# Kernel optimization log

Hardware: AMD Instinct MI355X
Metric: run time of the kernel (lower is better)

The kernel has to match this reference:

```python
import jax, jax.numpy as jnp
import numpy as np

N_NODES = 100000
N_EDGES = 6400000
IN_CH = 128
HID = 32


def setup_inputs() -> dict:
    key = jax.random.key(0)
    ks = jax.random.split(key, 12)
    x = jax.random.normal(ks[0], (N_NODES, IN_CH), dtype=jnp.float32)
    edge_index = jax.random.randint(ks[1], (2, N_EDGES), 0, N_NODES, dtype=jnp.int64)
    # Glorot-ish init for weights, zeros for biases (PyG / nn.Linear defaults vary,
    # values are random anyway for a correctness baseline)
    def w(k, fan_in, fan_out):
        s = 1.0 / np.sqrt(fan_in)
        return jax.random.uniform(k, (fan_in, fan_out), jnp.float32, -s, s)
    return {
        "x": x,
        "edge_index": edge_index,
        "W1": w(ks[2], IN_CH, HID), "b1": jnp.zeros((HID,), jnp.float32),
        "W2": w(ks[3], HID, HID),   "b2": jnp.zeros((HID,), jnp.float32),
        "Wl1": w(ks[4], HID, HID),  "bl1": jnp.zeros((HID,), jnp.float32),
        "Wl2": w(ks[5], HID, 1),    "bl2": jnp.zeros((1,), jnp.float32),
    }


def gcn_conv(x, W, b, src, dst, n_nodes):
    # GCNConv: h = x @ W; add self-loops; symmetric normalization D^-1/2 A_hat D^-1/2;
    # aggregate messages from src into dst; add bias.
    h = x @ W  # [N, out]
    loop = jnp.arange(n_nodes, dtype=src.dtype)
    src2 = jnp.concatenate([src, loop])
    dst2 = jnp.concatenate([dst, loop])
    ones = jnp.ones(src2.shape[0], dtype=h.dtype)
    deg = jax.ops.segment_sum(ones, dst2, num_segments=n_nodes)  # [N]
    dinv = jnp.where(deg > 0, jax.lax.rsqrt(deg), 0.0)
    norm = dinv[src2] * dinv[dst2]  # [E+N]
    msg = h[src2] * norm[:, None]   # [E+N, out]  (dominant memory traffic)
    out = jax.ops.segment_sum(msg, dst2, num_segments=n_nodes)
    return out + b


def reference(x, edge_index, W1, b1, W2, b2, Wl1, bl1, Wl2, bl2):
    src, dst = edge_index[0], edge_index[1]
    n = x.shape[0]
    h = jax.nn.relu(gcn_conv(x, W1, b1, src, dst, n))
    h = jax.nn.relu(gcn_conv(h, W2, b2, src, dst, n))
    h = jax.nn.relu(h @ Wl1 + bl1)
    return h @ Wl2 + bl2  # [N, 1]
```

## Files before the change

kernel.cpp:

```cpp
#include <hip/hip_runtime.h>

#define N_NODES 100000
#define N_EDGES 6400000
#define IN_CH   128
#define HID     32

#define BKT_SHIFT 9
#define BKT_MASK  511
#define BKT_SZ    512
#define NBKT      196
#define NBLK      1024
#define TILE      6250
#define QMAX      8704

#define O_EBUF 0u
#define O_HS   0u
#define O_HS2  12800000u
#define O_GH   25600000u
#define O_CUR  26402816u
#define O_CSR  26402816u
#define O_ROWS 52002816u
#define O_BST  52402824u
#define O_BTOT 52403616u
#define O_FLAG 52404400u

__global__ void k_detect(const unsigned int* e, int* flag) {
    __shared__ int any;
    if (threadIdx.x == 0) any = 0;
    __syncthreads();
    int acc = 0;
    for (int i = threadIdx.x; i < 4096; i += 256)
        acc |= (e[2 * i + 1] != 0u);
    if (acc) atomicOr(&any, 1);
    __syncthreads();
    if (threadIdx.x == 0) *flag = any ? 0 : 1;
}

__device__ __forceinline__ int eload_nt(const int* e, int is64, long long idx) {
    return is64 ? (int)__builtin_nontemporal_load((const long long*)e + idx)
                : __builtin_nontemporal_load(e + (size_t)idx);
}

__global__ void k_hist(const int* e, const int* flag, int* ghist) {
    __shared__ int h[NBKT];
    for (int i = threadIdx.x; i < NBKT; i += 256) h[i] = 0;
    __syncthreads();
    int is64 = *flag;
    long long base = (long long)blockIdx.x * TILE;
    for (int k = threadIdx.x; k < TILE; k += 256) {
        int dst = eload_nt(e, is64, (long long)N_EDGES + base + k);
        atomicAdd(&h[dst >> BKT_SHIFT], 1);
    }
    __syncthreads();
    int* g = ghist + blockIdx.x * NBKT;
    for (int i = threadIdx.x; i < NBKT; i += 256) g[i] = h[i];
}

__global__ void k_scan1(const int* __restrict__ ghist, int* __restrict__ btot) {
    int j = blockIdx.x;
    int t = threadIdx.x;
    int s = 0;
    for (int blk = t; blk < NBLK; blk += 64) s += ghist[blk * NBKT + j];
#pragma unroll
    for (int off = 32; off; off >>= 1) s += __shfl_down(s, off, 64);
    if (t == 0) btot[j] = s;
}

__global__ void k_scan2(const int* __restrict__ btot, int* __restrict__ bstart) {
    __shared__ int s[1024];
    int t = threadIdx.x;
    int v = (t < NBKT) ? btot[t] : 0;
    s[t] = v;
    __syncthreads();
    for (int off = 1; off < 1024; off <<= 1) {
        int u = (t >= off) ? s[t - off] : 0;
        __syncthreads();
        s[t] += u;
        __syncthreads();
    }
    if (t < NBKT) bstart[t] = s[t] - v;
    if (t == 0) bstart[NBKT] = N_EDGES;
}

__global__ void k_scan3(const int* __restrict__ ghist, const int* __restrict__ bstart,
                        int* __restrict__ cursors) {
    int j = blockIdx.x * 256 + threadIdx.x;
    if (j >= NBKT) return;
    int run = bstart[j];
    for (int blk = 0; blk < NBLK; ++blk) {
        cursors[blk * NBKT + j] = run;
        run += ghist[blk * NBKT + j];
    }
}

__launch_bounds__(512)
__global__ void k_scatter(const int* e, const int* flag,
                          const int* __restrict__ ghist, const int* __restrict__ cursors,
                          unsigned int* __restrict__ ebuf) {
    __shared__ unsigned obuf[TILE];
    __shared__ unsigned char bid[TILE];
    __shared__ int lcur[NBKT];
    __shared__ int gbase[NBKT];
    __shared__ int wsum[8];
    int t = threadIdx.x;
    int blk = blockIdx.x;
    {
        int v = (t < NBKT) ? ghist[blk * NBKT + t] : 0;
        int lane = t & 63, w = t >> 6;
        int p = v;
#pragma unroll
        for (int off = 1; off < 64; off <<= 1) {
            int u = __shfl_up(p, off, 64);
            if (lane >= off) p += u;
        }
        if (lane == 63) wsum[w] = p;
        __syncthreads();
        int woff = 0;
        for (int k = 0; k < w; ++k) woff += wsum[k];
        int excl = woff + p - v;
        if (t < NBKT) {
            lcur[t]  = excl;
            gbase[t] = cursors[blk * NBKT + t] - excl;
        }
    }
    __syncthreads();
    int is64 = *flag;
    long long base = (long long)blk * TILE;
    for (int k = t; k < TILE; k += 512) {
        int src = eload_nt(e, is64, base + k);
        int dst = eload_nt(e, is64, (long long)N_EDGES + base + k);
        int b = dst >> BKT_SHIFT;
        int pos = atomicAdd(&lcur[b], 1);
        obuf[pos] = ((unsigned)src << BKT_SHIFT) | (unsigned)(dst & BKT_MASK);
        bid[pos] = (unsigned char)b;
    }
    __syncthreads();
    for (int i = t; i < TILE; i += 512) {
        int b = bid[i];
        ebuf[gbase[b] + i] = obuf[i];
    }
}

__launch_bounds__(512)
__global__ void k_sort2a(const unsigned int* __restrict__ ebuf, const int* __restrict__ bstart,
                         unsigned short* __restrict__ gh2) {
    __shared__ int hist[BKT_SZ];
    int b = blockIdx.x >> 2, q = blockIdx.x & 3;
    int s0 = bstart[b], e0 = bstart[b + 1], len = e0 - s0;
    int lo = s0 + (int)((long long)len * q / 4);
    int hi = s0 + (int)((long long)len * (q + 1) / 4);
    hist[threadIdx.x] = 0;
    __syncthreads();
    for (int i = lo + (int)threadIdx.x; i < hi; i += 512)
        atomicAdd(&hist[__builtin_nontemporal_load(&ebuf[i]) & BKT_MASK], 1);
    __syncthreads();
    gh2[(b * 4 + q) * BKT_SZ + threadIdx.x] = (unsigned short)hist[threadIdx.x];
}

__launch_bounds__(512)
__global__ void k_sort2b(const unsigned int* __restrict__ ebuf, const int* __restrict__ bstart,
                         const unsigned short* __restrict__ gh2, int* __restrict__ csr,
                         int* __restrict__ rows) {
    __shared__ unsigned obuf[QMAX];
    __shared__ unsigned short bid[QMAX];
    __shared__ int lcur[BKT_SZ];
    __shared__ int gbase[BKT_SZ];
    __shared__ int wsA[8], wsB[8];
    int b = blockIdx.x >> 2, q = blockIdx.x & 3;
    int s0 = bstart[b], e0 = bstart[b + 1], len = e0 - s0;
    int lo = s0 + (int)((long long)len * q / 4);
    int hi = s0 + (int)((long long)len * (q + 1) / 4);
    int t = threadIdx.x;
    int h0 = gh2[(b * 4 + 0) * BKT_SZ + t];
    int h1 = gh2[(b * 4 + 1) * BKT_SZ + t];
    int h2 = gh2[(b * 4 + 2) * BKT_SZ + t];
    int h3 = gh2[(b * 4 + 3) * BKT_SZ + t];
    int tot = h0 + h1 + h2 + h3;
    int hq = (q == 0) ? h0 : (q == 1) ? h1 : (q == 2) ? h2 : h3;
    int lane = t & 63, w = t >> 6;
    int p1 = tot, p2 = hq;
#pragma unroll
    for (int off = 1; off < 64; off <<= 1) {
        int u1 = __shfl_up(p1, off, 64);
        int u2 = __shfl_up(p2, off, 64);
        if (lane >= off) { p1 += u1; p2 += u2; }
    }
    if (lane == 63) { wsA[w] = p1; wsB[w] = p2; }
    __syncthreads();
    int woffA = 0, woffB = 0;
    for (int k = 0; k < w; ++k) { woffA += wsA[k]; woffB += wsB[k]; }
    int binstart = s0 + woffA + p1 - tot;
    int lexcl    = woffB + p2 - hq;
    int qs = binstart + ((q > 0) ? h0 : 0) + ((q > 1) ? h1 : 0) + ((q > 2) ? h2 : 0);
    lcur[t]  = lexcl;
    gbase[t] = qs - lexcl;
    int node = b * BKT_SZ + t;
    if (q == 0 && node <= N_NODES) rows[node] = binstart;
    __syncthreads();
    for (int i = lo + t; i < hi; i += 512) {
        unsigned v = __builtin_nontemporal_load(&ebuf[i]);
        int bin = v & BKT_MASK;
        int pos = atomicAdd(&lcur[bin], 1);
        obuf[pos] = v >> BKT_SHIFT;
        bid[pos] = (unsigned short)bin;
    }
    __syncthreads();
    int qlen = hi - lo;
    for (int i = t; i < qlen; i += 512) {
        int bn = bid[i];
        csr[gbase[bn] + i] = (int)obuf[i];
    }
}

__launch_bounds__(256)
__global__ void k_gemm1(const float* __restrict__ x, const float* __restrict__ W1,
                        const int* __restrict__ rows, float* __restrict__ hs) {
    __shared__ float w[IN_CH * HID];
    __shared__ float xs[8 * IN_CH];
    for (int i = threadIdx.x; i < IN_CH * HID; i += 256) w[i] = W1[i];
    const float4* xb = (const float4*)(x + (size_t)blockIdx.x * 8 * IN_CH);
    ((float4*)xs)[threadIdx.x] = xb[threadIdx.x];
    __syncthreads();
    int lane = threadIdx.x & 31, hw = threadIdx.x >> 5;
    int node = blockIdx.x * 8 + hw;
    float dv = rsqrtf((float)(rows[node + 1] - rows[node] + 1));
    const float* xr = xs + hw * IN_CH;
    float acc = 0.f;
#pragma unroll
    for (int k = 0; k < IN_CH; ++k) acc += xr[k] * w[k * HID + lane];
    hs[(size_t)node * HID + lane] = acc * dv;
}

__device__ __forceinline__ float gather_row(const float* __restrict__ feat,
                                            const int* __restrict__ cs,
                                            int len, int lane, float acc) {
    int j = 0;
    for (; j + 16 <= len; j += 16) {
        int idx[16];
#pragma unroll
        for (int u = 0; u < 16; ++u) idx[u] = cs[j + u];
        float f[16];
#pragma unroll
        for (int u = 0; u < 16; ++u) f[u] = feat[(size_t)idx[u] * HID + lane];
        acc += (((f[0] + f[1]) + (f[2] + f[3])) + ((f[4] + f[5]) + (f[6] + f[7])))
             + (((f[8] + f[9]) + (f[10] + f[11])) + ((f[12] + f[13]) + (f[14] + f[15])));
    }
    for (; j + 8 <= len; j += 8) {
        int idx[8];
#pragma unroll
        for (int u = 0; u < 8; ++u) idx[u] = cs[j + u];
        float f[8];
#pragma unroll
        for (int u = 0; u < 8; ++u) f[u] = feat[(size_t)idx[u] * HID + lane];
        acc += ((f[0] + f[1]) + (f[2] + f[3])) + ((f[4] + f[5]) + (f[6] + f[7]));
    }
    for (; j < len; ++j) acc += feat[(size_t)cs[j] * HID + lane];
    return acc;
}

__launch_bounds__(256)
__global__ void k_agg1(const float* __restrict__ hs, const int* __restrict__ csr,
                       const int* __restrict__ rows, const float* __restrict__ b1,
                       const float* __restrict__ W2, float* __restrict__ hs2) {
    __shared__ float w2[HID * HID];
    __shared__ float h1s[8][HID];
    for (int i = threadIdx.x; i < HID * HID; i += 256) w2[i] = W2[i];
    int lane = threadIdx.x & 31, hw = threadIdx.x >> 5;
    int node = blockIdx.x * 8 + hw;
    int r0 = rows[node], r1 = rows[node + 1];
    float dv = rsqrtf((float)(r1 - r0 + 1));
    float acc = hs[(size_t)node * HID + lane];
    acc = gather_row(hs, csr + r0, r1 - r0, lane, acc);
    h1s[hw][lane] = fmaxf(acc * dv + b1[lane], 0.f);
    __syncthreads();
    float g = 0.f;
#pragma unroll
    for (int k = 0; k < HID; ++k) g += h1s[hw][k] * w2[k * HID + lane];
    hs2[(size_t)node * HID + lane] = g * dv;
}

__launch_bounds__(256)
__global__ void k_agg2(const float* __restrict__ hs2, const int* __restrict__ csr,
                       const int* __restrict__ rows, const float* __restrict__ b2,
                       const float* __restrict__ Wl1, const float* __restrict__ bl1,
                       const float* __restrict__ Wl2, const float* __restrict__ bl2,
                       float* __restrict__ out) {
    __shared__ float wl1[HID * HID];
    __shared__ float h2s[8][HID];
    for (int i = threadIdx.x; i < HID * HID; i += 256) wl1[i] = Wl1[i];
    int lane = threadIdx.x & 31, hw = threadIdx.x >> 5;
    int node = blockIdx.x * 8 + hw;
    int r0 = rows[node], r1 = rows[node + 1];
    float dv = rsqrtf((float)(r1 - r0 + 1));
    float acc = hs2[(size_t)node * HID + lane];
    acc = gather_row(hs2, csr + r0, r1 - r0, lane, acc);
    float h2 = fmaxf(acc * dv + b2[lane], 0.f);
    h2s[hw][lane] = h2;
    __syncthreads();
    float g = bl1[lane];
#pragma unroll
    for (int k = 0; k < HID; ++k) g += h2s[hw][k] * wl1[k * HID + lane];
    float o = fmaxf(g, 0.f) * Wl2[lane];
#pragma unroll
    for (int off = 16; off; off >>= 1) o += __shfl_down(o, off, 32);
    if (lane == 0) out[node] = o + *bl2;
}

extern "C" void kernel_launch(void* const* d_in, const int* in_sizes, int n_in,
                              void* d_out, int out_size, void* d_ws, size_t ws_size,
                              hipStream_t stream) {
    const float* x   = (const float*)d_in[0];
    const int*   e   = (const int*)d_in[1];
    const float* W1  = (const float*)d_in[2];
    const float* b1  = (const float*)d_in[3];
    const float* W2  = (const float*)d_in[4];
    const float* b2  = (const float*)d_in[5];
    const float* Wl1 = (const float*)d_in[6];
    const float* bl1 = (const float*)d_in[7];
    const float* Wl2 = (const float*)d_in[8];
    const float* bl2 = (const float*)d_in[9];
    float* out = (float*)d_out;

    char* w = (char*)d_ws;
    unsigned int*   ebuf    = (unsigned int*)(w + O_EBUF);
    float*          hs      = (float*)(w + O_HS);
    float*          hs2     = (float*)(w + O_HS2);
    int*            ghist   = (int*)(w + O_GH);
    unsigned short* gh2     = (unsigned short*)(w + O_GH);
    int*            cursors = (int*)(w + O_CUR);
    int*            csr     = (int*)(w + O_CSR);
    int*            rows    = (int*)(w + O_ROWS);
    int*            bstart  = (int*)(w + O_BST);
    int*            btot    = (int*)(w + O_BTOT);
    int*            flag    = (int*)(w + O_FLAG);

    const int NB_NODE = N_NODES / 8;

    k_detect<<<1, 256, 0, stream>>>((const unsigned int*)e, flag);
    k_hist<<<NBLK, 256, 0, stream>>>(e, flag, ghist);
    k_scan1<<<NBKT, 64, 0, stream>>>(ghist, btot);
    k_scan2<<<1, 1024, 0, stream>>>(btot, bstart);
    k_scan3<<<1, 256, 0, stream>>>(ghist, bstart, cursors);
    k_scatter<<<NBLK, 512, 0, stream>>>(e, flag, ghist, cursors, ebuf);
    k_sort2a<<<NBKT * 4, 512, 0, stream>>>(ebuf, bstart, gh2);
    k_sort2b<<<NBKT * 4, 512, 0, stream>>>(ebuf, bstart, gh2, csr, rows);

    k_gemm1<<<NB_NODE, 256, 0, stream>>>(x, W1, rows, hs);
    k_agg1<<<NB_NODE, 256, 0, stream>>>(hs, csr, rows, b1, W2, hs2);
    k_agg2<<<NB_NODE, 256, 0, stream>>>(hs2, csr, rows, b2,
                                        Wl1, bl1, Wl2, bl2, out);
}
```

Measured before the change: 373.8 us.

## Split aggregation into four 8-channel passes over quarter-sized feature tables

Feature matrices are now stored as four channel slices of 8 floats per node (3.2 MB each) instead of 32-float rows. Each aggregation runs four passes, one per slice, so the gathered table is small enough to stay cache-resident. Each pass uses 8 lanes per edge and 8 edges per wave, followed by a shuffle reduction. The GEMM stages are split out into separate kernels that write the sliced layout. The trade-off is that the CSR index array is read four times per layer, there are more kernel launches, and each gather is only 32 bytes wide.

```diff
diff --git a/kernel.cpp b/kernel.cpp
--- a/kernel.cpp
+++ b/kernel.cpp
@@ -4,6 +4,7 @@
 #define N_EDGES 6400000
 #define IN_CH   128
 #define HID     32
+#define QT      800000
 
 #define BKT_SHIFT 9
 #define BKT_MASK  511
@@ -14,8 +15,8 @@
 #define QMAX      8704
 
 #define O_EBUF 0u
-#define O_HS   0u
-#define O_HS2  12800000u
+#define O_A0   0u
+#define O_A1   12800000u
 #define O_GH   25600000u
 #define O_CUR  26402816u
 #define O_CSR  26402816u
@@ -214,9 +215,10 @@
 
 __launch_bounds__(256)
 __global__ void k_gemm1(const float* __restrict__ x, const float* __restrict__ W1,
-                        const int* __restrict__ rows, float* __restrict__ hs) {
+                        const int* __restrict__ rows, float* __restrict__ hsq) {
     __shared__ float w[IN_CH * HID];
     __shared__ float xs[8 * IN_CH];
+    __shared__ float hstage[8][HID];
     for (int i = threadIdx.x; i < IN_CH * HID; i += 256) w[i] = W1[i];
     const float4* xb = (const float4*)(x + (size_t)blockIdx.x * 8 * IN_CH);
     ((float4*)xs)[threadIdx.x] = xb[threadIdx.x];
@@ -228,74 +230,81 @@
     float acc = 0.f;
 #pragma unroll
     for (int k = 0; k < IN_CH; ++k) acc += xr[k] * w[k * HID + lane];
-    hs[(size_t)node * HID + lane] = acc * dv;
-}
-
-__device__ __forceinline__ float gather_row(const float* __restrict__ feat,
-                                            const int* __restrict__ cs,
-                                            int len, int lane, float acc) {
-    int j = 0;
-    for (; j + 16 <= len; j += 16) {
-        int idx[16];
-#pragma unroll
-        for (int u = 0; u < 16; ++u) idx[u] = cs[j + u];
-        float f[16];
-#pragma unroll
-        for (int u = 0; u < 16; ++u) f[u] = feat[(size_t)idx[u] * HID + lane];
-        acc += (((f[0] + f[1]) + (f[2] + f[3])) + ((f[4] + f[5]) + (f[6] + f[7])))
-             + (((f[8] + f[9]) + (f[10] + f[11])) + ((f[12] + f[13]) + (f[14] + f[15])));
-    }
-    for (; j + 8 <= len; j += 8) {
-        int idx[8];
-#pragma unroll
-        for (int u = 0; u < 8; ++u) idx[u] = cs[j + u];
-        float f[8];
-#pragma unroll
-        for (int u = 0; u < 8; ++u) f[u] = feat[(size_t)idx[u] * HID + lane];
-        acc += ((f[0] + f[1]) + (f[2] + f[3])) + ((f[4] + f[5]) + (f[6] + f[7]));
-    }
-    for (; j < len; ++j) acc += feat[(size_t)cs[j] * HID + lane];
-    return acc;
+    hstage[hw][lane] = acc * dv;
+    __syncthreads();
+    int q = threadIdx.x >> 6, k2 = threadIdx.x & 63;
+    hsq[(size_t)q * QT + blockIdx.x * 64 + k2] = hstage[k2 >> 3][q * 8 + (k2 & 7)];
+}
+
+__launch_bounds__(512)
+__global__ void k_aggpass(const float* __restrict__ tq, const int* __restrict__ csr,
+                          const int* __restrict__ rows, const float* __restrict__ bias,
+                          float* __restrict__ outq) {
+    __shared__ float stage[8][8];
+    int tid = threadIdx.x;
+    int wv = tid >> 6, lane = tid & 63;
+    int eg = lane >> 3, c = lane & 7;
+    int node = blockIdx.x * 8 + wv;
+    int r0 = rows[node], r1 = rows[node + 1];
+    float dv = rsqrtf((float)(r1 - r0 + 1));
+    float acc = 0.f;
+    int j = r0 + eg;
+    for (; j + 24 < r1; j += 32) {
+        int i0 = __builtin_nontemporal_load(csr + j);
+        int i1 = __builtin_nontemporal_load(csr + j + 8);
+        int i2 = __builtin_nontemporal_load(csr + j + 16);
+        int i3 = __builtin_nontemporal_load(csr + j + 24);
+        float f0 = tq[i0 * 8 + c];
+        float f1 = tq[i1 * 8 + c];
+        float f2 = tq[i2 * 8 + c];
+        float f3 = tq[i3 * 8 + c];
+        acc += (f0 + f1) + (f2 + f3);
+    }
+    for (; j < r1; j += 8)
+        acc += tq[__builtin_nontemporal_load(csr + j) * 8 + c];
+#pragma unroll
+    for (int off = 8; off < 64; off <<= 1)
+        acc += __shfl_xor(acc, off, 64);
+    acc += tq[node * 8 + c];
+    float v = fmaxf(acc * dv + bias[c], 0.f);
+    if (lane < 8) stage[wv][c] = v;
+    __syncthreads();
+    if (tid < 64)
+        __builtin_nontemporal_store(stage[tid >> 3][tid & 7],
+                                    outq + (size_t)blockIdx.x * 64 + tid);
 }
 
 __launch_bounds__(256)
-__global__ void k_agg1(const float* __restrict__ hs, const int* __restrict__ csr,
-                       const int* __restrict__ rows, const float* __restrict__ b1,
-                       const float* __restrict__ W2, float* __restrict__ hs2) {
+__global__ void k_gemm2(const float* __restrict__ h1q, const float* __restrict__ W2,
+                        const int* __restrict__ rows, float* __restrict__ hs2q) {
     __shared__ float w2[HID * HID];
     __shared__ float h1s[8][HID];
+    __shared__ float hstage[8][HID];
     for (int i = threadIdx.x; i < HID * HID; i += 256) w2[i] = W2[i];
     int lane = threadIdx.x & 31, hw = threadIdx.x >> 5;
     int node = blockIdx.x * 8 + hw;
-    int r0 = rows[node], r1 = rows[node + 1];
-    float dv = rsqrtf((float)(r1 - r0 + 1));
-    float acc = hs[(size_t)node * HID + lane];
-    acc = gather_row(hs, csr + r0, r1 - r0, lane, acc);
-    h1s[hw][lane] = fmaxf(acc * dv + b1[lane], 0.f);
-    __syncthreads();
+    h1s[hw][lane] = h1q[(size_t)(lane >> 3) * QT + node * 8 + (lane & 7)];
+    __syncthreads();
+    float dv = rsqrtf((float)(rows[node + 1] - rows[node] + 1));
     float g = 0.f;
 #pragma unroll
     for (int k = 0; k < HID; ++k) g += h1s[hw][k] * w2[k * HID + lane];
-    hs2[(size_t)node * HID + lane] = g * dv;
+    hstage[hw][lane] = g * dv;
+    __syncthreads();
+    int q = threadIdx.x >> 6, k2 = threadIdx.x & 63;
+    hs2q[(size_t)q * QT + blockIdx.x * 64 + k2] = hstage[k2 >> 3][q * 8 + (k2 & 7)];
 }
 
 __launch_bounds__(256)
-__global__ void k_agg2(const float* __restrict__ hs2, const int* __restrict__ csr,
-                       const int* __restrict__ rows, const float* __restrict__ b2,
-                       const float* __restrict__ Wl1, const float* __restrict__ bl1,
-                       const float* __restrict__ Wl2, const float* __restrict__ bl2,
-                       float* __restrict__ out) {
+__global__ void k_head(const float* __restrict__ h2q, const float* __restrict__ Wl1,
+                       const float* __restrict__ bl1, const float* __restrict__ Wl2,
+                       const float* __restrict__ bl2, float* __restrict__ out) {
     __shared__ float wl1[HID * HID];
     __shared__ float h2s[8][HID];
     for (int i = threadIdx.x; i < HID * HID; i += 256) wl1[i] = Wl1[i];
     int lane = threadIdx.x & 31, hw = threadIdx.x >> 5;
     int node = blockIdx.x * 8 + hw;
-    int r0 = rows[node], r1 = rows[node + 1];
-    float dv = rsqrtf((float)(r1 - r0 + 1));
-    float acc = hs2[(size_t)node * HID + lane];
-    acc = gather_row(hs2, csr + r0, r1 - r0, lane, acc);
-    float h2 = fmaxf(acc * dv + b2[lane], 0.f);
-    h2s[hw][lane] = h2;
+    h2s[hw][lane] = h2q[(size_t)(lane >> 3) * QT + node * 8 + (lane & 7)];
     __syncthreads();
     float g = bl1[lane];
 #pragma unroll
@@ -322,17 +331,17 @@
     float* out = (float*)d_out;
 
     char* w = (char*)d_ws;
-    unsigned int*   ebuf    = (unsigned int*)(w + O_EBUF);
-    float*          hs      = (float*)(w + O_HS);
-    float*          hs2     = (float*)(w + O_HS2);
-    int*            ghist   = (int*)(w + O_GH);
-    unsigned short* gh2     = (unsigned short*)(w + O_GH);
-    int*            cursors = (int*)(w + O_CUR);
-    int*            csr     = (int*)(w + O_CSR);
-    int*            rows    = (int*)(w + O_ROWS);
-    int*            bstart  = (int*)(w + O_BST);
-    int*            btot    = (int*)(w + O_BTOT);
-    int*            flag    = (int*)(w + O_FLAG);
+    unsigned int*   ebuf   = (unsigned int*)(w + O_EBUF);
+    float*          A0     = (float*)(w + O_A0);
+    float*          A1     = (float*)(w + O_A1);
+    int*            ghist  = (int*)(w + O_GH);
+    unsigned short* gh2    = (unsigned short*)(w + O_GH);
+    int*            cursors= (int*)(w + O_CUR);
+    int*            csr    = (int*)(w + O_CSR);
+    int*            rows   = (int*)(w + O_ROWS);
+    int*            bstart = (int*)(w + O_BST);
+    int*            btot   = (int*)(w + O_BTOT);
+    int*            flag   = (int*)(w + O_FLAG);
 
     const int NB_NODE = N_NODES / 8;
 
@@ -345,8 +354,13 @@
     k_sort2a<<<NBKT * 4, 512, 0, stream>>>(ebuf, bstart, gh2);
     k_sort2b<<<NBKT * 4, 512, 0, stream>>>(ebuf, bstart, gh2, csr, rows);
 
-    k_gemm1<<<NB_NODE, 256, 0, stream>>>(x, W1, rows, hs);
-    k_agg1<<<NB_NODE, 256, 0, stream>>>(hs, csr, rows, b1, W2, hs2);
-    k_agg2<<<NB_NODE, 256, 0, stream>>>(hs2, csr, rows, b2,
-                                        Wl1, bl1, Wl2, bl2, out);
-}
+    k_gemm1<<<NB_NODE, 256, 0, stream>>>(x, W1, rows, A0);
+    for (int q = 0; q < 4; ++q)
+        k_aggpass<<<NB_NODE, 512, 0, stream>>>(A0 + (size_t)q * QT, csr, rows,
+                                               b1 + 8 * q, A1 + (size_t)q * QT);
+    k_gemm2<<<NB_NODE, 256, 0, stream>>>(A1, W2, rows, A0);
+    for (int q = 0; q < 4; ++q)
+        k_aggpass<<<NB_NODE, 512, 0, stream>>>(A0 + (size_t)q * QT, csr, rows,
+                                               b2 + 8 * q, A1 + (size_t)q * QT);
+    k_head<<<NB_NODE, 256, 0, stream>>>(A1, Wl1, bl1, Wl2, bl2, out);
+}
```

Result: slower. 726.1 us (+94.2%).
